# Kernel optimization log

Hardware: AMD Instinct MI355X
Metric: run time of the kernel (lower is better)

## Reference

```python
import jax, jax.numpy as jnp
import numpy as np

N_NODES = 100000
N_EDGES = 1600000


def setup_inputs() -> dict:
    key = jax.random.key(0)
    ks = jax.random.split(key, 6)
    x = jax.random.normal(ks[0], (N_NODES, 128), dtype=jnp.float32)
    src = jax.random.randint(ks[1], (N_EDGES,), 0, N_NODES, dtype=jnp.int32)
    dst = jax.random.randint(ks[2], (N_EDGES,), 0, N_NODES, dtype=jnp.int32)
    # Glorot-ish scaled weights
    W1 = jax.random.normal(ks[3], (128, 64), dtype=jnp.float32) / np.sqrt(128.0)
    b1 = jnp.zeros((64,), dtype=jnp.float32)
    W2 = jax.random.normal(ks[4], (64, 64), dtype=jnp.float32) / np.sqrt(64.0)
    b2 = jnp.zeros((64,), dtype=jnp.float32)
    return {"x": x, "src": src, "dst": dst, "W1": W1, "b1": b1, "W2": W2, "b2": b2}


def _gcn_forward(x, src_f, dst_f, norm_src, norm_dst, W1, b1, W2, b2):
    n = x.shape[0]

    def conv(h, W, b):
        # weight-first (in_feats >= out_feats in DGL GraphConv): h W is cheap, aggregate small dim
        h = h @ W                                  # [N, d_out]
        h = h * norm_src[:, None]                  # D_out^{-1/2} on source side
        msg = h[src_f]                             # gather per edge [E+N, d_out]
        agg = jax.ops.segment_sum(msg, dst_f, num_segments=n)  # scatter-add to dst
        return agg * norm_dst[:, None] + b         # D_in^{-1/2} + bias

    h = jax.nn.relu(conv(x, W1, b1))
    return conv(h, W2, b2)


def reference(x, src, dst, W1, b1, W2, b2):
    n = x.shape[0]
    loop = jnp.arange(n, dtype=src.dtype)
    src_f = jnp.concatenate([src, loop])  # dgl.add_self_loop
    dst_f = jnp.concatenate([dst, loop])
    ones = jnp.ones(src_f.shape[0], dtype=x.dtype)
    out_deg = jax.ops.segment_sum(ones, src_f, num_segments=n)
    in_deg = jax.ops.segment_sum(ones, dst_f, num_segments=n)
    norm_src = jax.lax.rsqrt(out_deg)  # deg >= 1 due to self loops
    norm_dst = jax.lax.rsqrt(in_deg)
    return _gcn_forward(x, src_f, dst_f, norm_src, norm_dst, W1, b1, W2, b2)
```

## Files before the change

kernel.cpp:

```cpp
#include <hip/hip_runtime.h>
#include <hip/hip_fp16.h>

#define D 64
#define NBUCK 512
#define EPB 4096
#define SRC_BLOCKS 64
#define BDST 16
#define HWORDS 25088
#define BSTAGE 8192

typedef __attribute__((ext_vector_type(8))) short short8;
typedef __attribute__((ext_vector_type(4))) float floatx4;

__global__ __launch_bounds__(1024) void k_hist(const int* __restrict__ src,
                                               const int* __restrict__ dst,
                                               unsigned* __restrict__ hstage,
                                               int* __restrict__ bucket_cnt_part,
                                               int E, int N) {
    const int E4 = E >> 2;
    int tid = threadIdx.x;

    if (blockIdx.x < BDST) {
        __shared__ int hb[NBUCK];
        for (int i = tid; i < NBUCK; i += 1024) hb[i] = 0;
        __syncthreads();
        const int4* d4 = (const int4*)dst;
        int stride = BDST * 1024;
        for (int i = blockIdx.x * 1024 + tid; i < E4; i += stride) {
            int4 v = d4[i];
            atomicAdd(&hb[v.x >> 8], 1);
            atomicAdd(&hb[v.y >> 8], 1);
            atomicAdd(&hb[v.z >> 8], 1);
            atomicAdd(&hb[v.w >> 8], 1);
        }
        if (blockIdx.x == 0) {
            int e = E4 * 4 + tid;
            if (e < E) atomicAdd(&hb[dst[e] >> 8], 1);
        }
        __syncthreads();
        int* my = bucket_cnt_part + blockIdx.x * NBUCK;
        for (int i = tid; i < NBUCK; i += 1024) my[i] = hb[i];
    } else {
        __shared__ unsigned hw[HWORDS];
        int wlen = (N + 3) >> 2;
        for (int i = tid; i < wlen; i += 1024) hw[i] = 0;
        __syncthreads();
        const int4* s4 = (const int4*)src;
        int b = blockIdx.x - BDST;
        int stride = SRC_BLOCKS * 1024;
        for (int i = b * 1024 + tid; i < E4; i += stride) {
            int4 v = s4[i];
            atomicAdd(&hw[v.x >> 2], 1u << ((v.x & 3) * 8));
            atomicAdd(&hw[v.y >> 2], 1u << ((v.y & 3) * 8));
            atomicAdd(&hw[v.z >> 2], 1u << ((v.z & 3) * 8));
            atomicAdd(&hw[v.w >> 2], 1u << ((v.w & 3) * 8));
        }
        if (b == 0) {
            int e = E4 * 4 + tid;
            if (e < E) {
                int v = src[e];
                atomicAdd(&hw[v >> 2], 1u << ((v & 3) * 8));
            }
        }
        __syncthreads();
        unsigned* my = hstage + (long long)b * wlen;
        for (int i = tid; i < wlen; i += 1024) my[i] = hw[i];
    }
}

__global__ __launch_bounds__(512) void k_scanB(const int* __restrict__ bucket_cnt_part,
                                               int* __restrict__ bucket_ptr,
                                               int* __restrict__ row_ptr, int N, int E) {
    __shared__ int s[512];
    int tid = threadIdx.x;
    int v = 0;
#pragma unroll
    for (int b = 0; b < BDST; ++b) v += bucket_cnt_part[b * NBUCK + tid];
    s[tid] = v;
    __syncthreads();
    for (int off = 1; off < 512; off <<= 1) {
        int add = (tid >= off) ? s[tid - off] : 0;
        __syncthreads();
        s[tid] += add;
        __syncthreads();
    }
    bucket_ptr[tid] = s[tid] - v;
    if (tid == 511) bucket_ptr[512] = s[511];
    if (tid == 0) row_ptr[N] = E;
}

__global__ __launch_bounds__(256) void k_bin(const int* __restrict__ src,
                                             const int* __restrict__ dst,
                                             const int* __restrict__ bucket_ptr,
                                             int* __restrict__ bucket_cursor,
                                             unsigned long long* __restrict__ binned,
                                             int E) {
    __shared__ int cnt[NBUCK];
    __shared__ int bloc[NBUCK];
    __shared__ int lcur[NBUCK];
    __shared__ int gbase[NBUCK];
    __shared__ int ss[256];
    __shared__ unsigned long long stage[EPB];

    int tid = threadIdx.x;
    int start = blockIdx.x * EPB;
    int nloc = min(EPB, E - start);

    for (int i = tid; i < NBUCK; i += 256) cnt[i] = 0;
    __syncthreads();

#pragma unroll
    for (int r = 0; r < EPB / 256; ++r) {
        int idx = start + r * 256 + tid;
        if (idx < E) atomicAdd(&cnt[dst[idx] >> 8], 1);
    }
    __syncthreads();

    int a = cnt[2 * tid], b = cnt[2 * tid + 1];
    ss[tid] = a + b;
    __syncthreads();
    for (int off = 1; off < 256; off <<= 1) {
        int add = (tid >= off) ? ss[tid - off] : 0;
        __syncthreads();
        ss[tid] += add;
        __syncthreads();
    }
    int excl = ss[tid] - (a + b);
    bloc[2 * tid] = excl;           lcur[2 * tid] = excl;
    bloc[2 * tid + 1] = excl + a;   lcur[2 * tid + 1] = excl + a;
    __syncthreads();

    for (int bk = tid; bk < NBUCK; bk += 256) {
        int c = cnt[bk];
        gbase[bk] = c ? (atomicAdd(&bucket_cursor[bk], c) + bucket_ptr[bk]) : 0;
    }
    __syncthreads();

#pragma unroll
    for (int r = 0; r < EPB / 256; ++r) {
        int idx = start + r * 256 + tid;
        if (idx < E) {
            int d = dst[idx];
            int p = atomicAdd(&lcur[d >> 8], 1);
            stage[p] = ((unsigned long long)(unsigned)d << 32) | (unsigned)src[idx];
        }
    }
    __syncthreads();

#pragma unroll
    for (int r = 0; r < EPB / 256; ++r) {
        int i = r * 256 + tid;
        if (i < nloc) {
            unsigned long long e = stage[i];
            int bk = (int)(e >> 40);
            binned[gbase[bk] + (i - bloc[bk])] = e;
        }
    }
}

__global__ __launch_bounds__(256) void k_bsort(const unsigned long long* __restrict__ binned,
                                               const int* __restrict__ bucket_ptr,
                                               const unsigned* __restrict__ hstage,
                                               int* __restrict__ csr,
                                               int* __restrict__ row_ptr,
                                               float* __restrict__ norm_src,
                                               float* __restrict__ norm_dst, int N) {
    __shared__ unsigned long long est[BSTAGE];
    __shared__ int cnt256[256];
    __shared__ int ss[256];
    __shared__ int cur[256];
    int b = blockIdx.x;
    int n0 = b << 8;
    int tid = threadIdx.x;
    int base = bucket_ptr[b];
    int ctot = bucket_ptr[b + 1] - base;
    bool fits = (ctot <= BSTAGE);

    cnt256[tid] = 0;
    __syncthreads();

    if (fits) {
        for (int k = tid; k < ctot; k += 256) {
            unsigned long long e = binned[base + k];
            est[k] = e;
            atomicAdd(&cnt256[(int)(e >> 32) - n0], 1);
        }
    } else {
        for (int k = tid; k < ctot; k += 256)
            atomicAdd(&cnt256[(int)(binned[base + k] >> 32) - n0], 1);
    }
    __syncthreads();

    int v = cnt256[tid];
    ss[tid] = v;
    __syncthreads();
    for (int off = 1; off < 256; off <<= 1) {
        int add = (tid >= off) ? ss[tid - off] : 0;
        __syncthreads();
        ss[tid] += add;
        __syncthreads();
    }
    int excl = ss[tid] - v;
    int node = n0 + tid;
    if (node < N) {
        row_ptr[node] = base + excl;
        norm_dst[node] = rsqrtf((float)v + 1.0f);
        int wlen = (N + 3) >> 2;
        unsigned sh = (unsigned)(node & 3) * 8u;
        const unsigned* q = hstage + (node >> 2);
        int od = 0;
#pragma unroll 8
        for (int p = 0; p < SRC_BLOCKS; ++p) {
            od += (int)((*q >> sh) & 0xffu);
            q += wlen;
        }
        norm_src[node] = rsqrtf((float)od + 1.0f);
    }
    cur[tid] = base + excl;
    __syncthreads();

    if (fits) {
        for (int k = tid; k < ctot; k += 256) {
            unsigned long long e = est[k];
            int p = atomicAdd(&cur[(int)(e >> 32) - n0], 1);
            csr[p] = (int)(e & 0xffffffffu);
        }
    } else {
        for (int k = tid; k < ctot; k += 256) {
            unsigned long long e = binned[base + k];
            int p = atomicAdd(&cur[(int)(e >> 32) - n0], 1);
            csr[p] = (int)(e & 0xffffffffu);
        }
    }
}

template <int K>
__global__ __launch_bounds__(256) void k_gemm_mfma(const float* __restrict__ hsrc,
                                                   const float* __restrict__ W,
                                                   const float* __restrict__ norm_src,
                                                   __half* __restrict__ t, int N) {
    constexpr int NKI = K / 32;
    __shared__ short Whi[NKI * 2048];
    __shared__ short Wlo[NKI * 2048];
    int tid = threadIdx.x;

    for (int f = tid; f < K * 64; f += 256) {
        int n  = f & 15;
        int j  = (f >> 4) & 7;
        int q  = (f >> 7) & 3;
        int ct = (f >> 9) & 3;
        int ki = f >> 11;
        int k = ki * 32 + q * 8 + j;
        int c = ct * 16 + n;
        float w = W[k * 64 + c];
        unsigned u = __float_as_uint(w);
        float l = w - __uint_as_float(u & 0xffff0000u);
        int idx = (((ki * 4 + ct) * 16 + n) * 4 + q) * 8 + j;
        Whi[idx] = (short)(u >> 16);
        Wlo[idx] = (short)(__float_as_uint(l) >> 16);
    }
    __syncthreads();

    int wave = tid >> 6, lane = tid & 63;
    int q = lane >> 4, n = lane & 15;
    int r0 = blockIdx.x * 64 + wave * 16;
    int rowc = min(r0 + n, N - 1);

    floatx4 acc[4] = {{0.f,0.f,0.f,0.f},{0.f,0.f,0.f,0.f},
                      {0.f,0.f,0.f,0.f},{0.f,0.f,0.f,0.f}};

    for (int ki = 0; ki < NKI; ++ki) {
        const float* ap = hsrc + (long long)rowc * K + ki * 32 + q * 8;
        float4 a0 = *(const float4*)ap;
        float4 a1 = *(const float4*)(ap + 4);
        float av[8] = {a0.x, a0.y, a0.z, a0.w, a1.x, a1.y, a1.z, a1.w};
        short8 ahi, alo;
#pragma unroll
        for (int j = 0; j < 8; ++j) {
            unsigned u = __float_as_uint(av[j]);
            float l = av[j] - __uint_as_float(u & 0xffff0000u);
            ahi[j] = (short)(u >> 16);
            alo[j] = (short)(__float_as_uint(l) >> 16);
        }
#pragma unroll
        for (int ct = 0; ct < 4; ++ct) {
            int bidx = (((ki * 4 + ct) * 16 + n) * 4 + q) * 8;
            short8 bhi = *(const short8*)&Whi[bidx];
            short8 blo = *(const short8*)&Wlo[bidx];
            acc[ct] = __builtin_amdgcn_mfma_f32_16x16x32_bf16(ahi, bhi, acc[ct], 0, 0, 0);
            acc[ct] = __builtin_amdgcn_mfma_f32_16x16x32_bf16(ahi, blo, acc[ct], 0, 0, 0);
            acc[ct] = __builtin_amdgcn_mfma_f32_16x16x32_bf16(alo, bhi, acc[ct], 0, 0, 0);
        }
    }

#pragma unroll
    for (int reg = 0; reg < 4; ++reg) {
        int orow = r0 + q * 4 + reg;
        if (orow < N) {
            float nrm = norm_src[orow];
#pragma unroll
            for (int ct = 0; ct < 4; ++ct)
                t[(long long)orow * 64 + ct * 16 + n] = __float2half(acc[ct][reg] * nrm);
        }
    }
}

__global__ __launch_bounds__(256) void k_agg(const int* __restrict__ row_ptr,
                                             const int* __restrict__ csr,
                                             const __half* __restrict__ t,
                                             const float* __restrict__ norm_dst,
                                             const float* __restrict__ bias,
                                             float* __restrict__ out, int N, int do_relu) {
    int tid = threadIdx.x;
    int half_id = tid >> 5;
    int lane = tid & 31;
    int i = blockIdx.x * 8 + half_id;
    if (i >= N) return;
    const __half2* t2 = (const __half2*)t;
    int start = row_ptr[i];
    int c = row_ptr[i + 1] - start;

    float2 sf = __half22float2(t2[i * 32 + lane]);
    float ax = sf.x, ay = sf.y;

    int j = 0;
    int pre = min(c, (4 - (start & 3)) & 3);
    for (; j < pre; ++j) {
        float2 f = __half22float2(t2[csr[start + j] * 32 + lane]);
        ax += f.x; ay += f.y;
    }
    for (; j + 16 <= c; j += 16) {
        int4 s4 = *(const int4*)&csr[start + j];
        int4 s5 = *(const int4*)&csr[start + j + 4];
        int4 s6 = *(const int4*)&csr[start + j + 8];
        int4 s7 = *(const int4*)&csr[start + j + 12];
        float2 f0 = __half22float2(t2[s4.x * 32 + lane]);
        float2 f1 = __half22float2(t2[s4.y * 32 + lane]);
        float2 f2 = __half22float2(t2[s4.z * 32 + lane]);
        float2 f3 = __half22float2(t2[s4.w * 32 + lane]);
        float2 f4 = __half22float2(t2[s5.x * 32 + lane]);
        float2 f5 = __half22float2(t2[s5.y * 32 + lane]);
        float2 f6 = __half22float2(t2[s5.z * 32 + lane]);
        float2 f7 = __half22float2(t2[s5.w * 32 + lane]);
        float2 f8 = __half22float2(t2[s6.x * 32 + lane]);
        float2 f9 = __half22float2(t2[s6.y * 32 + lane]);
        float2 fa = __half22float2(t2[s6.z * 32 + lane]);
        float2 fb = __half22float2(t2[s6.w * 32 + lane]);
        float2 fc = __half22float2(t2[s7.x * 32 + lane]);
        float2 fd = __half22float2(t2[s7.y * 32 + lane]);
        float2 fe = __half22float2(t2[s7.z * 32 + lane]);
        float2 ff = __half22float2(t2[s7.w * 32 + lane]);
        ax += (((f0.x + f1.x) + (f2.x + f3.x)) + ((f4.x + f5.x) + (f6.x + f7.x)))
            + (((f8.x + f9.x) + (fa.x + fb.x)) + ((fc.x + fd.x) + (fe.x + ff.x)));
        ay += (((f0.y + f1.y) + (f2.y + f3.y)) + ((f4.y + f5.y) + (f6.y + f7.y)))
            + (((f8.y + f9.y) + (fa.y + fb.y)) + ((fc.y + fd.y) + (fe.y + ff.y)));
    }
    for (; j + 8 <= c; j += 8) {
        int4 s4 = *(const int4*)&csr[start + j];
        int4 s5 = *(const int4*)&csr[start + j + 4];
        float2 f0 = __half22float2(t2[s4.x * 32 + lane]);
        float2 f1 = __half22float2(t2[s4.y * 32 + lane]);
        float2 f2 = __half22float2(t2[s4.z * 32 + lane]);
        float2 f3 = __half22float2(t2[s4.w * 32 + lane]);
        float2 f4 = __half22float2(t2[s5.x * 32 + lane]);
        float2 f5 = __half22float2(t2[s5.y * 32 + lane]);
        float2 f6 = __half22float2(t2[s5.z * 32 + lane]);
        float2 f7 = __half22float2(t2[s5.w * 32 + lane]);
        ax += ((f0.x + f1.x) + (f2.x + f3.x)) + ((f4.x + f5.x) + (f6.x + f7.x));
        ay += ((f0.y + f1.y) + (f2.y + f3.y)) + ((f4.y + f5.y) + (f6.y + f7.y));
    }
    for (; j + 4 <= c; j += 4) {
        int4 s4 = *(const int4*)&csr[start + j];
        float2 f0 = __half22float2(t2[s4.x * 32 + lane]);
        float2 f1 = __half22float2(t2[s4.y * 32 + lane]);
        float2 f2 = __half22float2(t2[s4.z * 32 + lane]);
        float2 f3 = __half22float2(t2[s4.w * 32 + lane]);
        ax += (f0.x + f1.x) + (f2.x + f3.x);
        ay += (f0.y + f1.y) + (f2.y + f3.y);
    }
    for (; j < c; ++j) {
        float2 f = __half22float2(t2[csr[start + j] * 32 + lane]);
        ax += f.x; ay += f.y;
    }

    float nrm = norm_dst[i];
    float2 bb = ((const float2*)bias)[lane];
    float vx = fmaf(ax, nrm, bb.x);
    float vy = fmaf(ay, nrm, bb.y);
    if (do_relu) { vx = fmaxf(vx, 0.f); vy = fmaxf(vy, 0.f); }
    float2 o; o.x = vx; o.y = vy;
    ((float2*)out)[i * 32 + lane] = o;
}

extern "C" void kernel_launch(void* const* d_in, const int* in_sizes, int n_in,
                              void* d_out, int out_size, void* d_ws, size_t ws_size,
                              hipStream_t stream) {
    const float* x   = (const float*)d_in[0];
    const int*   src = (const int*)d_in[1];
    const int*   dst = (const int*)d_in[2];
    const float* W1  = (const float*)d_in[3];
    const float* b1  = (const float*)d_in[4];
    const float* W2  = (const float*)d_in[5];
    const float* b2  = (const float*)d_in[6];
    float* out = (float*)d_out;

    const int N = in_sizes[0] / 128;
    const int E = in_sizes[1];

    int*   bucket_cursor  = (int*)d_ws;
    int*   bucket_cnt_part= bucket_cursor + 512;
    int*   bucket_ptr     = bucket_cnt_part + BDST * NBUCK;
    int*   row_ptr        = bucket_ptr + 513;
    float* norm_src       = (float*)(row_ptr + N + 1);
    float* norm_dst       = norm_src + N;
    long long toff = (3LL * N + 512 + BDST * NBUCK + 514 + 63) & ~63LL;
    float* tbase    = (float*)d_ws + toff;
    float* h        = tbase + (long long)N * 32;
    int*   csr      = (int*)(h + (long long)N * D);
    __half* t_h = (__half*)tbase;
    unsigned long long* binned = (unsigned long long*)tbase;
    unsigned* hstage = (unsigned*)h;

    const int NB = (N + 255) / 256;
    const int NBK = (E + EPB - 1) / EPB;

    hipMemsetAsync(bucket_cursor, 0, 512 * sizeof(int), stream);

    k_hist<<<BDST + SRC_BLOCKS, 1024, 0, stream>>>(src, dst, hstage, bucket_cnt_part, E, N);
    k_scanB<<<1, 512, 0, stream>>>(bucket_cnt_part, bucket_ptr, row_ptr, N, E);
    k_bin<<<NBK, 256, 0, stream>>>(src, dst, bucket_ptr, bucket_cursor, binned, E);
    k_bsort<<<NB, 256, 0, stream>>>(binned, bucket_ptr, hstage, csr, row_ptr,
                                    norm_src, norm_dst, N);

    k_gemm_mfma<128><<<(N + 63) / 64, 256, 0, stream>>>(x, W1, norm_src, t_h, N);
    k_agg<<<(N + 7) / 8, 256, 0, stream>>>(row_ptr, csr, t_h, norm_dst, b1, h, N, 1);

    k_gemm_mfma<64><<<(N + 63) / 64, 256, 0, stream>>>(h, W2, norm_src, t_h, N);
    k_agg<<<(N + 7) / 8, 256, 0, stream>>>(row_ptr, csr, t_h, norm_dst, b2, out, N, 0);
}
```

Before: 276.8 us.

## Move source-degree histogram into binning kernel, split by node halves

The source out-degree histogram moves out of the first histogram kernel and into extra blocks of the binning kernel, reusing its shared staging buffer. It is split into two node halves across 128 blocks, so each block's shared histogram is half the size. The dst histogram gets more blocks, EPB doubles to 8192, and the 16-way unrolled gather loop in aggregation is removed. The goal is to overlap the src histogram with binning and raise occupancy, at the cost of each block reading all src edges and filtering by range.

New measurement: 284.2 us. 2.7% more time.

```diff
diff --git a/kernel.cpp b/kernel.cpp
--- a/kernel.cpp
+++ b/kernel.cpp
@@ -3,69 +3,38 @@
 
 #define D 64
 #define NBUCK 512
-#define EPB 4096
-#define SRC_BLOCKS 64
-#define BDST 16
-#define HWORDS 25088
+#define EPB 8192
+#define BDST 32
+#define NSH 128
 #define BSTAGE 8192
 
 typedef __attribute__((ext_vector_type(8))) short short8;
 typedef __attribute__((ext_vector_type(4))) float floatx4;
 
-__global__ __launch_bounds__(1024) void k_hist(const int* __restrict__ src,
-                                               const int* __restrict__ dst,
-                                               unsigned* __restrict__ hstage,
-                                               int* __restrict__ bucket_cnt_part,
-                                               int E, int N) {
+__global__ __launch_bounds__(1024) void k_histdst(const int* __restrict__ dst,
+                                                  int* __restrict__ bucket_cnt_part,
+                                                  int E) {
+    __shared__ int hb[NBUCK];
+    int tid = threadIdx.x;
     const int E4 = E >> 2;
-    int tid = threadIdx.x;
-
-    if (blockIdx.x < BDST) {
-        __shared__ int hb[NBUCK];
-        for (int i = tid; i < NBUCK; i += 1024) hb[i] = 0;
-        __syncthreads();
-        const int4* d4 = (const int4*)dst;
-        int stride = BDST * 1024;
-        for (int i = blockIdx.x * 1024 + tid; i < E4; i += stride) {
-            int4 v = d4[i];
-            atomicAdd(&hb[v.x >> 8], 1);
-            atomicAdd(&hb[v.y >> 8], 1);
-            atomicAdd(&hb[v.z >> 8], 1);
-            atomicAdd(&hb[v.w >> 8], 1);
-        }
-        if (blockIdx.x == 0) {
-            int e = E4 * 4 + tid;
-            if (e < E) atomicAdd(&hb[dst[e] >> 8], 1);
-        }
-        __syncthreads();
-        int* my = bucket_cnt_part + blockIdx.x * NBUCK;
-        for (int i = tid; i < NBUCK; i += 1024) my[i] = hb[i];
-    } else {
-        __shared__ unsigned hw[HWORDS];
-        int wlen = (N + 3) >> 2;
-        for (int i = tid; i < wlen; i += 1024) hw[i] = 0;
-        __syncthreads();
-        const int4* s4 = (const int4*)src;
-        int b = blockIdx.x - BDST;
-        int stride = SRC_BLOCKS * 1024;
-        for (int i = b * 1024 + tid; i < E4; i += stride) {
-            int4 v = s4[i];
-            atomicAdd(&hw[v.x >> 2], 1u << ((v.x & 3) * 8));
-            atomicAdd(&hw[v.y >> 2], 1u << ((v.y & 3) * 8));
-            atomicAdd(&hw[v.z >> 2], 1u << ((v.z & 3) * 8));
-            atomicAdd(&hw[v.w >> 2], 1u << ((v.w & 3) * 8));
-        }
-        if (b == 0) {
-            int e = E4 * 4 + tid;
-            if (e < E) {
-                int v = src[e];
-                atomicAdd(&hw[v >> 2], 1u << ((v & 3) * 8));
-            }
-        }
-        __syncthreads();
-        unsigned* my = hstage + (long long)b * wlen;
-        for (int i = tid; i < wlen; i += 1024) my[i] = hw[i];
-    }
+    for (int i = tid; i < NBUCK; i += 1024) hb[i] = 0;
+    __syncthreads();
+    const int4* d4 = (const int4*)dst;
+    int stride = BDST * 1024;
+    for (int i = blockIdx.x * 1024 + tid; i < E4; i += stride) {
+        int4 v = d4[i];
+        atomicAdd(&hb[v.x >> 8], 1);
+        atomicAdd(&hb[v.y >> 8], 1);
+        atomicAdd(&hb[v.z >> 8], 1);
+        atomicAdd(&hb[v.w >> 8], 1);
+    }
+    if (blockIdx.x == 0) {
+        int e = E4 * 4 + tid;
+        if (e < E) atomicAdd(&hb[dst[e] >> 8], 1);
+    }
+    __syncthreads();
+    int* my = bucket_cnt_part + blockIdx.x * NBUCK;
+    for (int i = tid; i < NBUCK; i += 1024) my[i] = hb[i];
 }
 
 __global__ __launch_bounds__(512) void k_scanB(const int* __restrict__ bucket_cnt_part,
@@ -89,20 +58,54 @@
     if (tid == 0) row_ptr[N] = E;
 }
 
-__global__ __launch_bounds__(256) void k_bin(const int* __restrict__ src,
-                                             const int* __restrict__ dst,
-                                             const int* __restrict__ bucket_ptr,
-                                             int* __restrict__ bucket_cursor,
-                                             unsigned long long* __restrict__ binned,
-                                             int E) {
+__global__ __launch_bounds__(256) void k_binhist(const int* __restrict__ src,
+                                                 const int* __restrict__ dst,
+                                                 const int* __restrict__ bucket_ptr,
+                                                 int* __restrict__ bucket_cursor,
+                                                 unsigned long long* __restrict__ binned,
+                                                 unsigned* __restrict__ hstage,
+                                                 int E, int N, int NBK) {
+    __shared__ unsigned long long stage[EPB];
     __shared__ int cnt[NBUCK];
     __shared__ int bloc[NBUCK];
     __shared__ int lcur[NBUCK];
     __shared__ int gbase[NBUCK];
     __shared__ int ss[256];
-    __shared__ unsigned long long stage[EPB];
-
-    int tid = threadIdx.x;
+    int tid = threadIdx.x;
+    const int E4 = E >> 2;
+
+    if ((int)blockIdx.x >= NBK) {
+        unsigned* hw = (unsigned*)stage;
+        int b  = blockIdx.x - NBK;
+        int hb = b >> 6;
+        int c  = b & 63;
+        int NH = (N + 1) >> 1;
+        int lo = hb * NH;
+        int hi = min(lo + NH, N);
+        int wlen2 = (NH + 3) >> 2;
+        for (int i = tid; i < wlen2; i += 256) hw[i] = 0;
+        __syncthreads();
+        const int4* s4 = (const int4*)src;
+        for (int i = c * 256 + tid; i < E4; i += 64 * 256) {
+            int4 v = s4[i];
+            if (v.x >= lo && v.x < hi) { int l = v.x - lo; atomicAdd(&hw[l >> 2], 1u << ((l & 3) * 8)); }
+            if (v.y >= lo && v.y < hi) { int l = v.y - lo; atomicAdd(&hw[l >> 2], 1u << ((l & 3) * 8)); }
+            if (v.z >= lo && v.z < hi) { int l = v.z - lo; atomicAdd(&hw[l >> 2], 1u << ((l & 3) * 8)); }
+            if (v.w >= lo && v.w < hi) { int l = v.w - lo; atomicAdd(&hw[l >> 2], 1u << ((l & 3) * 8)); }
+        }
+        if (c == 0) {
+            int e = E4 * 4 + tid;
+            if (e < E) {
+                int v = src[e];
+                if (v >= lo && v < hi) { int l = v - lo; atomicAdd(&hw[l >> 2], 1u << ((l & 3) * 8)); }
+            }
+        }
+        __syncthreads();
+        unsigned* my = hstage + (long long)b * wlen2;
+        for (int i = tid; i < wlen2; i += 256) my[i] = hw[i];
+        return;
+    }
+
     int start = blockIdx.x * EPB;
     int nloc = min(EPB, E - start);
 
@@ -205,14 +208,17 @@
     if (node < N) {
         row_ptr[node] = base + excl;
         norm_dst[node] = rsqrtf((float)v + 1.0f);
-        int wlen = (N + 3) >> 2;
-        unsigned sh = (unsigned)(node & 3) * 8u;
-        const unsigned* q = hstage + (node >> 2);
+        int NH = (N + 1) >> 1;
+        int wlen2 = (NH + 3) >> 2;
+        int hb = (node >= NH) ? 1 : 0;
+        int local = node - hb * NH;
+        unsigned sh = (unsigned)(local & 3) * 8u;
+        const unsigned* q = hstage + (long long)(hb * 64) * wlen2 + (local >> 2);
         int od = 0;
 #pragma unroll 8
-        for (int p = 0; p < SRC_BLOCKS; ++p) {
+        for (int p = 0; p < 64; ++p) {
             od += (int)((*q >> sh) & 0xffu);
-            q += wlen;
+            q += wlen2;
         }
         norm_src[node] = rsqrtf((float)od + 1.0f);
     }
@@ -329,32 +335,6 @@
         float2 f = __half22float2(t2[csr[start + j] * 32 + lane]);
         ax += f.x; ay += f.y;
     }
-    for (; j + 16 <= c; j += 16) {
-        int4 s4 = *(const int4*)&csr[start + j];
-        int4 s5 = *(const int4*)&csr[start + j + 4];
-        int4 s6 = *(const int4*)&csr[start + j + 8];
-        int4 s7 = *(const int4*)&csr[start + j + 12];
-        float2 f0 = __half22float2(t2[s4.x * 32 + lane]);
-        float2 f1 = __half22float2(t2[s4.y * 32 + lane]);
-        float2 f2 = __half22float2(t2[s4.z * 32 + lane]);
-        float2 f3 = __half22float2(t2[s4.w * 32 + lane]);
-        float2 f4 = __half22float2(t2[s5.x * 32 + lane]);
-        float2 f5 = __half22float2(t2[s5.y * 32 + lane]);
-        float2 f6 = __half22float2(t2[s5.z * 32 + lane]);
-        float2 f7 = __half22float2(t2[s5.w * 32 + lane]);
-        float2 f8 = __half22float2(t2[s6.x * 32 + lane]);
-        float2 f9 = __half22float2(t2[s6.y * 32 + lane]);
-        float2 fa = __half22float2(t2[s6.z * 32 + lane]);
-        float2 fb = __half22float2(t2[s6.w * 32 + lane]);
-        float2 fc = __half22float2(t2[s7.x * 32 + lane]);
-        float2 fd = __half22float2(t2[s7.y * 32 + lane]);
-        float2 fe = __half22float2(t2[s7.z * 32 + lane]);
-        float2 ff = __half22float2(t2[s7.w * 32 + lane]);
-        ax += (((f0.x + f1.x) + (f2.x + f3.x)) + ((f4.x + f5.x) + (f6.x + f7.x)))
-            + (((f8.x + f9.x) + (fa.x + fb.x)) + ((fc.x + fd.x) + (fe.x + ff.x)));
-        ay += (((f0.y + f1.y) + (f2.y + f3.y)) + ((f4.y + f5.y) + (f6.y + f7.y)))
-            + (((f8.y + f9.y) + (fa.y + fb.y)) + ((fc.y + fd.y) + (fe.y + ff.y)));
-    }
     for (; j + 8 <= c; j += 8) {
         int4 s4 = *(const int4*)&csr[start + j];
         int4 s5 = *(const int4*)&csr[start + j + 4];
@@ -426,9 +406,10 @@
 
     hipMemsetAsync(bucket_cursor, 0, 512 * sizeof(int), stream);
 
-    k_hist<<<BDST + SRC_BLOCKS, 1024, 0, stream>>>(src, dst, hstage, bucket_cnt_part, E, N);
+    k_histdst<<<BDST, 1024, 0, stream>>>(dst, bucket_cnt_part, E);
     k_scanB<<<1, 512, 0, stream>>>(bucket_cnt_part, bucket_ptr, row_ptr, N, E);
-    k_bin<<<NBK, 256, 0, stream>>>(src, dst, bucket_ptr, bucket_cursor, binned, E);
+    k_binhist<<<NBK + NSH, 256, 0, stream>>>(src, dst, bucket_ptr, bucket_cursor,
+                                             binned, hstage, E, N, NBK);
     k_bsort<<<NB, 256, 0, stream>>>(binned, bucket_ptr, hstage, csr, row_ptr,
                                     norm_src, norm_dst, N);
 
```
